# Performance work log

Measured on AMD Instinct MI355X. Metric: run time of the kernel, lower is better.

The kernel has to match this reference:

```python
import jax, jax.numpy as jnp
import numpy as np

_LEVELS = jnp.array([-4, -2, -1, 0, 1, 2, 4], dtype=jnp.int32)  # shift-quant 7-value grid 'A'

B, S = 1, 512
IN_F, OUT_F = 4096, 16384
BLOCK = 64
NUM_BLOCKS = (IN_F + BLOCK - 1) // BLOCK  # 64


def setup_inputs() -> dict:
    key = jax.random.key(0)
    k1, k2, k3, k4 = jax.random.split(key, 4)
    x = jax.random.normal(k1, (B, S, IN_F), dtype=jnp.float32)
    idx = jax.random.randint(k2, (OUT_F, IN_F), 0, 7)
    q_weight = _LEVELS[idx]  # int32 values in {-4,-2,-1,0,1,2,4}
    scales = (jax.random.uniform(k3, (OUT_F, NUM_BLOCKS), dtype=jnp.float32) * 0.05 + 0.001).astype(jnp.float16)
    bias = (jax.random.normal(k4, (OUT_F,), dtype=jnp.float32) * 0.02).astype(jnp.float16)
    return {"x": x, "q_weight": q_weight, "scales": scales, "bias": bias, "block_size": BLOCK}


def reference(x, q_weight, scales, bias, block_size):
    # shift_matmul: dequantize blockwise-scaled power-of-two int8 weights, then GEMM.
    out_f, in_f = q_weight.shape
    # broadcast per-block fp16 scales along the in_features axis (handles padding block)
    w_scale = jnp.repeat(scales.astype(jnp.float32), block_size, axis=1)[:, :in_f]  # [out, in]
    w = q_weight.astype(jnp.float32) * w_scale  # [out, in]
    out = jnp.einsum("bsi,oi->bso", x, w)
    out = out + bias.astype(out.dtype)
    return out.astype(x.dtype)
```

## Files before the change

### kernel.cpp

```cpp
#include <hip/hip_runtime.h>
#include <hip/hip_bf16.h>
#include <stdint.h>


#define MM 512
#define NN 16384
#define KK 4096
#define BN 64
#define BK 128
#define NKB (KK / BK)

typedef __bf16 bf16x8 __attribute__((ext_vector_type(8)));
typedef float floatx4 __attribute__((ext_vector_type(4)));

__device__ __forceinline__ unsigned int pk_bf16_rtn(float lo, float hi) {
    __hip_bfloat162 h = __float22bfloat162_rn(float2{lo, hi});
    return *reinterpret_cast<unsigned int*>(&h);
}

__global__ __launch_bounds__(256) void pack_x(const float* __restrict__ x,
                                              unsigned short* __restrict__ xp) {
    const int t    = blockIdx.x * 256 + threadIdx.x;
    const int lane = t & 63;
    const int mt   = (t >> 6) & 31;
    const int ks   = (t >> 11) & 3;
    const int kb   = t >> 13;
    const int m    = mt * 16 + (lane & 15);
    const int k    = kb * 128 + ks * 32 + (lane >> 4) * 8;
    const float* px = x + (size_t)m * KK + k;
    const float4 a = *(const float4*)px;
    const float4 b = *(const float4*)(px + 4);
    uint4 o;
    o.x = pk_bf16_rtn(a.x, a.y);
    o.y = pk_bf16_rtn(a.z, a.w);
    o.z = pk_bf16_rtn(b.x, b.y);
    o.w = pk_bf16_rtn(b.z, b.w);
    *(uint4*)(xp + (size_t)t * 8) = o;
}

template <bool PRE>
__global__ __launch_bounds__(1024, 4) void qlin_gemm(
    const float* __restrict__ xf,
    const unsigned short* __restrict__ xp,
    const int* __restrict__ qw,
    const float* __restrict__ scales,
    const float* __restrict__ bias,
    float* __restrict__ out)
{
    __shared__ unsigned short sB[2][BN * BK];

    const int t    = threadIdx.x;
    const int lane = t & 63;
    const int w    = t >> 6;
    const int ln   = lane & 15;
    const int quad = lane >> 4;
    const int n0   = blockIdx.x * BN;

    const int brow = t >> 4;
    const int bk4  = (t & 15) * 4;
    const int* qp0 = qw + (size_t)(n0 + brow) * KK + bk4;
    const int* qp1 = qp0 + 64;
    const float2* sp = (const float2*)(scales + (size_t)(n0 + brow) * 64);

    floatx4 acc[2][4];
#pragma unroll
    for (int i = 0; i < 2; ++i)
#pragma unroll
        for (int j = 0; j < 4; ++j)
            acc[i][j] = (floatx4)0.0f;

    int4 qv0 = *(const int4*)(qp0);
    int4 qv1 = *(const int4*)(qp1);
    float2 ss = sp[0];

    for (int kb = 0; kb < NKB; ++kb) {
        unsigned short* sb = sB[kb & 1];
        uint2 u0, u1;
        u0.x = pk_bf16_rtn((float)qv0.x * ss.x, (float)qv0.y * ss.x);
        u0.y = pk_bf16_rtn((float)qv0.z * ss.x, (float)qv0.w * ss.x);
        u1.x = pk_bf16_rtn((float)qv1.x * ss.y, (float)qv1.y * ss.y);
        u1.y = pk_bf16_rtn((float)qv1.z * ss.y, (float)qv1.w * ss.y);
        *(uint2*)(sb + brow * BK + bk4)      = u0;
        *(uint2*)(sb + brow * BK + 64 + bk4) = u1;

        if (kb + 1 < NKB) {
            qv0 = *(const int4*)(qp0 + (size_t)(kb + 1) * BK);
            qv1 = *(const int4*)(qp1 + (size_t)(kb + 1) * BK);
            ss  = sp[kb + 1];
        }

        __syncthreads();

        const unsigned short* xpb = xp + (size_t)kb * (4 * 32 * 64 * 8);
#pragma unroll
        for (int ks = 0; ks < 4; ++ks) {
            bf16x8 a0, a1;
            if constexpr (PRE) {
                const unsigned short* ap = xpb + (size_t)((ks * 32 + w * 2) * 64 + lane) * 8;
                a0 = *(const bf16x8*)(ap);
                a1 = *(const bf16x8*)(ap + 64 * 8);
            } else {
                const int k = kb * BK + ks * 32 + quad * 8;
#pragma unroll
                for (int i = 0; i < 2; ++i) {
                    const float* px = xf + (size_t)(w * 32 + i * 16 + ln) * KK + k;
                    const float4 f0 = *(const float4*)px;
                    const float4 f1 = *(const float4*)(px + 4);
                    uint4 ua;
                    ua.x = pk_bf16_rtn(f0.x, f0.y);
                    ua.y = pk_bf16_rtn(f0.z, f0.w);
                    ua.z = pk_bf16_rtn(f1.x, f1.y);
                    ua.w = pk_bf16_rtn(f1.z, f1.w);
                    if (i == 0) a0 = *(bf16x8*)&ua; else a1 = *(bf16x8*)&ua;
                }
            }
            bf16x8 bfr[4];
#pragma unroll
            for (int j = 0; j < 4; ++j)
                bfr[j] = *(const bf16x8*)(sb + (j * 16 + ln) * BK + ks * 32 + quad * 8);
#pragma unroll
            for (int j = 0; j < 4; ++j) {
                acc[0][j] = __builtin_amdgcn_mfma_f32_16x16x32_bf16(a0, bfr[j], acc[0][j], 0, 0, 0);
                acc[1][j] = __builtin_amdgcn_mfma_f32_16x16x32_bf16(a1, bfr[j], acc[1][j], 0, 0, 0);
            }
        }
    }

#pragma unroll
    for (int j = 0; j < 4; ++j) {
        const int n = n0 + j * 16 + ln;
        const float bv = bias[n];
#pragma unroll
        for (int i = 0; i < 2; ++i) {
            const int mbase = w * 32 + i * 16 + quad * 4;
#pragma unroll
            for (int r = 0; r < 4; ++r)
                out[(size_t)(mbase + r) * NN + n] = acc[i][j][r] + bv;
        }
    }
}

extern "C" void kernel_launch(void* const* d_in, const int* in_sizes, int n_in,
                              void* d_out, int out_size, void* d_ws, size_t ws_size,
                              hipStream_t stream) {
    const float* x    = (const float*)d_in[0];
    const int* qw     = (const int*)d_in[1];
    const float* scl  = (const float*)d_in[2];
    const float* bias = (const float*)d_in[3];
    float* out        = (float*)d_out;

    dim3 grid(NN / BN);
    dim3 block(1024);

    if (ws_size >= (size_t)MM * KK * sizeof(unsigned short)) {
        unsigned short* xp = (unsigned short*)d_ws;
        pack_x<<<dim3(MM * KK / (256 * 8)), dim3(256), 0, stream>>>(x, xp);
        qlin_gemm<true><<<grid, block, 0, stream>>>(x, xp, qw, scl, bias, out);
    } else {
        qlin_gemm<false><<<grid, block, 0, stream>>>(x, nullptr, qw, scl, bias, out);
    }
}
```

Measured before the change: 454.0 us.

## Store dequantized weights in MFMA-fragment order with XOR swizzle and batch A loads

Each thread now loads 8 contiguous int32 weights and writes one 16-byte LDS store into a fragment-ordered, XOR-swizzled shared layout, so B fragments are read as contiguous per-lane 16-byte chunks. This targets LDS bank conflicts and the extra store instructions of the old row-major layout. All four k-step A fragments are loaded before the MFMA loop to hide global latency. The trade-off is higher register pressure under the 1024-thread launch bound, plus a per-thread scale index that changes with the thread's octet.

```diff
diff --git a/kernel.cpp b/kernel.cpp
--- a/kernel.cpp
+++ b/kernel.cpp
@@ -56,11 +56,14 @@
     const int quad = lane >> 4;
     const int n0   = blockIdx.x * BN;
 
-    const int brow = t >> 4;
-    const int bk4  = (t & 15) * 4;
-    const int* qp0 = qw + (size_t)(n0 + brow) * KK + bk4;
-    const int* qp1 = qp0 + 64;
-    const float2* sp = (const float2*)(scales + (size_t)(n0 + brow) * 64);
+    const int r    = t >> 4;
+    const int oct  = t & 15;
+    const int ksp  = oct >> 2;
+    const int jp   = r >> 4;
+    const int ldst = (((oct & 3) << 4) + (r & 15)) ^ (ksp << 1);
+    const int woff = ((ksp * 4 + jp) * 64 + ldst) * 8;
+    const int* qp  = qw + (size_t)(n0 + r) * KK + oct * 8;
+    const float* sp = scales + (size_t)(n0 + r) * 64 + (oct >> 3);
 
     floatx4 acc[2][4];
 #pragma unroll
@@ -69,36 +72,35 @@
         for (int j = 0; j < 4; ++j)
             acc[i][j] = (floatx4)0.0f;
 
-    int4 qv0 = *(const int4*)(qp0);
-    int4 qv1 = *(const int4*)(qp1);
-    float2 ss = sp[0];
+    int4 qv0 = *(const int4*)(qp);
+    int4 qv1 = *(const int4*)(qp + 4);
+    float s  = sp[0];
 
     for (int kb = 0; kb < NKB; ++kb) {
         unsigned short* sb = sB[kb & 1];
-        uint2 u0, u1;
-        u0.x = pk_bf16_rtn((float)qv0.x * ss.x, (float)qv0.y * ss.x);
-        u0.y = pk_bf16_rtn((float)qv0.z * ss.x, (float)qv0.w * ss.x);
-        u1.x = pk_bf16_rtn((float)qv1.x * ss.y, (float)qv1.y * ss.y);
-        u1.y = pk_bf16_rtn((float)qv1.z * ss.y, (float)qv1.w * ss.y);
-        *(uint2*)(sb + brow * BK + bk4)      = u0;
-        *(uint2*)(sb + brow * BK + 64 + bk4) = u1;
+        uint4 u;
+        u.x = pk_bf16_rtn((float)qv0.x * s, (float)qv0.y * s);
+        u.y = pk_bf16_rtn((float)qv0.z * s, (float)qv0.w * s);
+        u.z = pk_bf16_rtn((float)qv1.x * s, (float)qv1.y * s);
+        u.w = pk_bf16_rtn((float)qv1.z * s, (float)qv1.w * s);
+        *(uint4*)(sb + woff) = u;
 
         if (kb + 1 < NKB) {
-            qv0 = *(const int4*)(qp0 + (size_t)(kb + 1) * BK);
-            qv1 = *(const int4*)(qp1 + (size_t)(kb + 1) * BK);
-            ss  = sp[kb + 1];
+            qv0 = *(const int4*)(qp + (size_t)(kb + 1) * BK);
+            qv1 = *(const int4*)(qp + (size_t)(kb + 1) * BK + 4);
+            s   = sp[(size_t)(kb + 1) * 2];
         }
 
         __syncthreads();
 
+        bf16x8 a[4][2];
         const unsigned short* xpb = xp + (size_t)kb * (4 * 32 * 64 * 8);
 #pragma unroll
         for (int ks = 0; ks < 4; ++ks) {
-            bf16x8 a0, a1;
             if constexpr (PRE) {
                 const unsigned short* ap = xpb + (size_t)((ks * 32 + w * 2) * 64 + lane) * 8;
-                a0 = *(const bf16x8*)(ap);
-                a1 = *(const bf16x8*)(ap + 64 * 8);
+                a[ks][0] = *(const bf16x8*)(ap);
+                a[ks][1] = *(const bf16x8*)(ap + 512);
             } else {
                 const int k = kb * BK + ks * 32 + quad * 8;
 #pragma unroll
@@ -111,17 +113,20 @@
                     ua.y = pk_bf16_rtn(f0.z, f0.w);
                     ua.z = pk_bf16_rtn(f1.x, f1.y);
                     ua.w = pk_bf16_rtn(f1.z, f1.w);
-                    if (i == 0) a0 = *(bf16x8*)&ua; else a1 = *(bf16x8*)&ua;
+                    a[ks][i] = *(bf16x8*)&ua;
                 }
             }
+        }
+#pragma unroll
+        for (int ks = 0; ks < 4; ++ks) {
             bf16x8 bfr[4];
 #pragma unroll
             for (int j = 0; j < 4; ++j)
-                bfr[j] = *(const bf16x8*)(sb + (j * 16 + ln) * BK + ks * 32 + quad * 8);
+                bfr[j] = *(const bf16x8*)(sb + ((ks * 4 + j) * 64 + (lane ^ (ks << 1))) * 8);
 #pragma unroll
             for (int j = 0; j < 4; ++j) {
-                acc[0][j] = __builtin_amdgcn_mfma_f32_16x16x32_bf16(a0, bfr[j], acc[0][j], 0, 0, 0);
-                acc[1][j] = __builtin_amdgcn_mfma_f32_16x16x32_bf16(a1, bfr[j], acc[1][j], 0, 0, 0);
+                acc[0][j] = __builtin_amdgcn_mfma_f32_16x16x32_bf16(a[ks][0], bfr[j], acc[0][j], 0, 0, 0);
+                acc[1][j] = __builtin_amdgcn_mfma_f32_16x16x32_bf16(a[ks][1], bfr[j], acc[1][j], 0, 0, 0);
             }
         }
     }
@@ -134,8 +139,8 @@
         for (int i = 0; i < 2; ++i) {
             const int mbase = w * 32 + i * 16 + quad * 4;
 #pragma unroll
-            for (int r = 0; r < 4; ++r)
-                out[(size_t)(mbase + r) * NN + n] = acc[i][j][r] + bv;
+            for (int rr = 0; rr < 4; ++rr)
+                out[(size_t)(mbase + rr) * NN + n] = acc[i][j][rr] + bv;
         }
     }
 }
```

Measured after the change: 421.6 us. 1.08x faster.
